# Optimization experiments

Measured on AMD Instinct MI355X. Metric: run time of the kernel, lower is better.

The kernel has to match this reference:

```python
import jax, jax.numpy as jnp
import numpy as np

N, K, NC = 1024, 32, 10
CH = (1, 4, 8, 32)
FT = (256, 64, 16, 1)
BN_EPS = 1e-5

def _sgnroot(a):
    return jnp.sign(a) * jnp.maximum(jnp.sqrt(jnp.abs(a)), 1e-8)

def _row_normalize(a):
    y = a / (jnp.sum(jnp.abs(a), -1, keepdims=True) + 1e-7)
    return jnp.where(jnp.isnan(y), 0.0, y)

def _feature_adjacency(x, nbr):
    # x: [N,C,F], nbr: [N,K,C,F] -> adj: [N,C,F,F]
    a = jnp.einsum('ncx,nkcy->ncxy', x, nbr)
    a = a + jnp.swapaxes(a, -1, -2)
    return _row_normalize(_sgnroot(a))

def _transform(x, nbr, adj, W, b, oc, of):
    # aggregate with feature adjacency, then full-width Conv1d == dense contraction
    xa = jnp.einsum('ncxy,ncy->ncx', adj, x)          # [N,C,F]
    na = jnp.einsum('ncxy,nkcy->nkcx', adj, nbr)      # [N,K,C,F]
    xo = (jnp.einsum('ncf,dcf->nd', xa, W) + b).reshape(-1, oc, of)
    no = (jnp.einsum('nkcf,dcf->nkd', na, W) + b).reshape(xo.shape[0], -1, oc, of)
    return xo, no

def _bn_softsign(v, g, be, m, var):
    # BatchNorm1d (inference, running stats) over channel axis -2, then Softsign
    h = (v - m[:, None]) * jax.lax.rsqrt(var[:, None] + BN_EPS) * g[:, None] + be[:, None]
    return h / (1.0 + jnp.abs(h))

def setup_inputs():
    key = jax.random.key(0)
    ks = jax.random.split(key, 24)
    def rn(i, shape, s=1.0):
        return jax.random.normal(ks[i], shape, dtype=jnp.float32) * s
    return {
        'x': rn(0, (N, CH[0], FT[0])),
        'neighbor': rn(1, (N, K, CH[0], FT[0])),
        'W1': rn(2, (CH[1] * FT[1], CH[0], FT[0]), 0.05), 'b1': rn(3, (CH[1] * FT[1],), 0.05),
        'g1': jnp.ones((CH[1],), jnp.float32), 'be1': jnp.zeros((CH[1],), jnp.float32),
        'm1': rn(4, (CH[1],), 0.1), 'v1': jax.random.uniform(ks[5], (CH[1],), jnp.float32) + 0.5,
        'W2': rn(6, (CH[2] * FT[2], CH[1], FT[1]), 0.05), 'b2': rn(7, (CH[2] * FT[2],), 0.05),
        'g2': jnp.ones((CH[2],), jnp.float32), 'be2': jnp.zeros((CH[2],), jnp.float32),
        'm2': rn(8, (CH[2],), 0.1), 'v2': jax.random.uniform(ks[9], (CH[2],), jnp.float32) + 0.5,
        'W3': rn(10, (CH[3] * FT[3], CH[2], FT[2]), 0.05), 'b3': rn(11, (CH[3] * FT[3],), 0.05),
        'g3': jnp.ones((CH[3],), jnp.float32), 'be3': jnp.zeros((CH[3],), jnp.float32),
        'm3': rn(12, (CH[3],), 0.1), 'v3': jax.random.uniform(ks[13], (CH[3],), jnp.float32) + 0.5,
        'Wc': rn(14, (NC, CH[3] * FT[3]), 0.1), 'bc': rn(15, (NC,), 0.1),
    }

def reference(x, neighbor, W1, b1, g1, be1, m1, v1, W2, b2, g2, be2, m2, v2,
              W3, b3, g3, be3, m3, v3, Wc, bc):
    adj = _feature_adjacency(x, neighbor)
    x, neighbor = _transform(x, neighbor, adj, W1, b1, CH[1], FT[1])
    x, neighbor = _bn_softsign(x, g1, be1, m1, v1), _bn_softsign(neighbor, g1, be1, m1, v1)
    adj = _feature_adjacency(x, neighbor)
    x, neighbor = _transform(x, neighbor, adj, W2, b2, CH[2], FT[2])
    x, neighbor = _bn_softsign(x, g2, be2, m2, v2), _bn_softsign(neighbor, g2, be2, m2, v2)
    adj = _feature_adjacency(x, neighbor)
    x, _ = _transform(x, neighbor, adj, W3, b3, CH[3], FT[3])
    x = _bn_softsign(x, g3, be3, m3, v3)
    return x.reshape(N, -1) @ Wc.T + bc
```

## Files before the change

kernel.cpp:

```cpp
#include <hip/hip_runtime.h>
#include <cstddef>

#define NPT 1024
#define KNB 32
#define NR  33

typedef __attribute__((ext_vector_type(8))) _Float16 half8v;
typedef __attribute__((ext_vector_type(4))) float float4v;
typedef __attribute__((ext_vector_type(2))) float float2v;

union fragU { unsigned u[4]; half8v v; };
union f4u { float4 f4; float2v f2[2]; };

__global__ __launch_bounds__(256) void wconv_kernel(
        const float* __restrict__ W1, const float* __restrict__ W2,
        _Float16* __restrict__ W1f, _Float16* __restrict__ W2f) {
    int idx = blockIdx.x * 256 + threadIdx.x;
    if (idx < 65536) W1f[idx] = (_Float16)W1[idx];
    else if (idx < 65536 + 32768) W2f[idx - 65536] = (_Float16)W2[idx - 65536];
}

template<int F>
__device__ __forceinline__ void agg_phase(
        const _Float16 (*Rh)[264], _Float16 (*Nh)[264],
        const float* Xs, const float* Ss, int wv, int lane) {
    const int nbase = wv * 64;
    const int kch = (nbase / F) * F;
    const int l15 = lane & 15, lg = lane >> 4;

    float Xn[4], Sn[4];
    #pragma unroll
    for (int i = 0; i < 4; ++i) {
        int col = nbase + i * 16 + l15;
        Xn[i] = Xs[col]; Sn[i] = Ss[col];
    }

    float4v acc[3][4] = {};
    float rn[4] = {0.f, 0.f, 0.f, 0.f};

    const int KT = F / 32;
    for (int kt = 0; kt < KT; ++kt) {
        const int k0 = kch + kt * 32 + lg * 8;
        half8v af[3];
        af[0] = *reinterpret_cast<const half8v*>(&Rh[l15][k0]);
        af[1] = *reinterpret_cast<const half8v*>(&Rh[16 + l15][k0]);
        af[2] = half8v{};
        if (l15 == 0)
            af[2] = *reinterpret_cast<const half8v*>(&Rh[32][k0]);
        f4u xa0, xa1, sa0, sa1;
        xa0.f4 = *reinterpret_cast<const float4*>(&Xs[k0]);
        xa1.f4 = *reinterpret_cast<const float4*>(&Xs[k0 + 4]);
        sa0.f4 = *reinterpret_cast<const float4*>(&Ss[k0]);
        sa1.f4 = *reinterpret_cast<const float4*>(&Ss[k0 + 4]);
        const float2v xk2[4] = {xa0.f2[0], xa0.f2[1], xa1.f2[0], xa1.f2[1]};
        const float2v sk2[4] = {sa0.f2[0], sa0.f2[1], sa1.f2[0], sa1.f2[1]};
        #pragma unroll
        for (int ni = 0; ni < 4; ++ni) {
            const float xn = Xn[ni], sn = Sn[ni];
            fragU bf;
            float2v rloc2 = {0.f, 0.f};
            #pragma unroll
            for (int jj = 0; jj < 4; ++jj) {
                const float2v a = xn * sk2[jj] + xk2[jj] * sn;
                const float r0 = __builtin_amdgcn_sqrtf(__builtin_fabsf(a.x));
                const float r1 = __builtin_amdgcn_sqrtf(__builtin_fabsf(a.y));
                rloc2 += (float2v){r0, r1};
                const unsigned mag = __builtin_bit_cast(unsigned,
                    __builtin_amdgcn_cvt_pkrtz(r0, r1));
                const unsigned sgn = __builtin_bit_cast(unsigned,
                    __builtin_amdgcn_cvt_pkrtz(a.x, a.y)) & 0x80008000u;
                bf.u[jj] = mag | sgn;
            }
            rn[ni] += rloc2.x + rloc2.y;
            #pragma unroll
            for (int m = 0; m < 3; ++m)
                acc[m][ni] = __builtin_amdgcn_mfma_f32_16x16x32_f16(
                                 af[m], bf.v, acc[m][ni], 0, 0, 0);
        }
    }

    #pragma unroll
    for (int ni = 0; ni < 4; ++ni) {
        rn[ni] += __shfl_xor(rn[ni], 16);
        rn[ni] += __shfl_xor(rn[ni], 32);
        rn[ni] = __builtin_amdgcn_rcpf(rn[ni] + 1e-7f);
    }

    #pragma unroll
    for (int m = 0; m < 3; ++m) {
        const int rbase = m * 16 + (lg << 2);
        #pragma unroll
        for (int ni = 0; ni < 4; ++ni) {
            const int col = nbase + ni * 16 + l15;
            #pragma unroll
            for (int i = 0; i < 4; ++i) {
                int r = rbase + i;
                if (r < NR)
                    Nh[r][col] = (_Float16)(acc[m][ni][i] * rn[ni]);
            }
        }
    }
}

template<int DOUT, int FP>
__device__ __forceinline__ void proj_phase(
        const _Float16 (*Nh)[264], _Float16 (*Rh)[264],
        float* Xs, float* Ss,
        const _Float16* __restrict__ Wf,
        const float* __restrict__ bias,
        const float* __restrict__ g, const float* __restrict__ be,
        const float* __restrict__ m, const float* __restrict__ var,
        int wv, int lane) {
    const int l15 = lane & 15, lg = lane >> 4;
    constexpr int NTW = DOUT / 64;
    const int nbase = wv * (NTW * 16);

    float4v acc[3][NTW] = {};

    for (int kt = 0; kt < 8; ++kt) {
        const int k0 = kt * 32 + lg * 8;
        half8v ah[3];
        ah[0] = *reinterpret_cast<const half8v*>(&Nh[l15][k0]);
        ah[1] = *reinterpret_cast<const half8v*>(&Nh[16 + l15][k0]);
        ah[2] = half8v{};
        if (l15 == 0)
            ah[2] = *reinterpret_cast<const half8v*>(&Nh[32][k0]);
        #pragma unroll
        for (int ni = 0; ni < NTW; ++ni) {
            const int d = nbase + ni * 16 + l15;
            const half8v bh = *reinterpret_cast<const half8v*>(Wf + (size_t)d * 256 + k0);
            #pragma unroll
            for (int mi = 0; mi < 3; ++mi)
                acc[mi][ni] = __builtin_amdgcn_mfma_f32_16x16x32_f16(
                                  ah[mi], bh, acc[mi][ni], 0, 0, 0);
        }
    }

    #pragma unroll
    for (int ni = 0; ni < NTW; ++ni) {
        const int col = nbase + ni * 16 + l15;
        const int c = (nbase + ni * 16) / FP;
        const float sc = g[c] * __builtin_amdgcn_rsqf(var[c] + 1e-5f);
        const float hb = (bias[col] - m[c]) * sc + be[c];
        float colsum = 0.f, xval = 0.f;
        #pragma unroll
        for (int mi = 0; mi < 3; ++mi) {
            const int rbase = mi * 16 + (lg << 2);
            #pragma unroll
            for (int i = 0; i < 4; ++i) {
                const int r = rbase + i;
                if (r < NR) {
                    float h = acc[mi][ni][i] * sc + hb;
                    h = h * __builtin_amdgcn_rcpf(1.f + __builtin_fabsf(h));
                    Rh[r][col] = (_Float16)h;
                    if (r < 32) colsum += h; else xval = h;
                }
            }
        }
        colsum += __shfl_xor(colsum, 16);
        colsum += __shfl_xor(colsum, 32);
        if (lg == 0) { Ss[col] = colsum; Xs[col] = xval; }
    }
}

__global__ __launch_bounds__(256, 4) void fused_kernel(
        const float* __restrict__ x, const float* __restrict__ nbr,
        const _Float16* __restrict__ W1f, const float* __restrict__ b1,
        const float* __restrict__ g1, const float* __restrict__ be1,
        const float* __restrict__ m1, const float* __restrict__ v1,
        const _Float16* __restrict__ W2f, const float* __restrict__ b2,
        const float* __restrict__ g2, const float* __restrict__ be2,
        const float* __restrict__ m2, const float* __restrict__ v2,
        const float* __restrict__ W3, const float* __restrict__ b3,
        const float* __restrict__ g3, const float* __restrict__ be3,
        const float* __restrict__ m3, const float* __restrict__ v3,
        const float* __restrict__ Wc, const float* __restrict__ bc,
        float* __restrict__ out) {
    const int n_pt = blockIdx.x, t = threadIdx.x;
    const int lane = t & 63, wv = t >> 6;

    __shared__ __align__(16) _Float16 Rh[NR][264];
    __shared__ __align__(16) _Float16 Nh[NR][264];
    __shared__ __align__(16) float Xs[256], Ss[256];
    __shared__ float xa3[128], hs3[32];

    {
        const float* nb = nbr + (size_t)n_pt * (KNB * 256);
        float s = 0.f;
        #pragma unroll 4
        for (int k = 0; k < KNB; ++k) {
            float v = nb[k * 256 + t];
            Rh[k][t] = (_Float16)v;
            s += v;
        }
        Ss[t] = s;
        float xv = x[(size_t)n_pt * 256 + t];
        Rh[32][t] = (_Float16)xv;
        Xs[t] = xv;
    }
    __syncthreads();

    agg_phase<256>(Rh, Nh, Xs, Ss, wv, lane);
    __syncthreads();
    proj_phase<256, 64>(Nh, Rh, Xs, Ss, W1f, b1, g1, be1, m1, v1, wv, lane);
    __syncthreads();

    agg_phase<64>(Rh, Nh, Xs, Ss, wv, lane);
    __syncthreads();
    proj_phase<128, 16>(Nh, Rh, Xs, Ss, W2f, b2, g2, be2, m2, v2, wv, lane);
    __syncthreads();

    if (t < 128) {
        const int base = (t >> 4) << 4;
        const float xv = Xs[t], sv = Ss[t];
        float racc = 0.f, acc = 0.f;
        #pragma unroll
        for (int y = 0; y < 16; ++y) {
            const float xy = Xs[base + y];
            const float a = xv * Ss[base + y] + xy * sv;
            const float r = __builtin_amdgcn_sqrtf(__builtin_fabsf(a));
            racc += r;
            acc += __builtin_copysignf(r, a) * xy;
        }
        xa3[t] = acc * __builtin_amdgcn_rcpf(racc + 1e-7f);
    }
    __syncthreads();

    if (t < 32) {
        const float* w = W3 + (size_t)t * 128;
        float acc = b3[t];
        #pragma unroll 4
        for (int i = 0; i < 128; ++i) acc += w[i] * xa3[i];
        float h = (acc - m3[t]) * __builtin_amdgcn_rsqf(v3[t] + 1e-5f) * g3[t] + be3[t];
        hs3[t] = h * __builtin_amdgcn_rcpf(1.f + __builtin_fabsf(h));
    }
    __syncthreads();

    if (t < 10) {
        const float* w = Wc + (size_t)t * 32;
        float acc = bc[t];
        #pragma unroll
        for (int i = 0; i < 32; ++i) acc += w[i] * hs3[i];
        out[(size_t)n_pt * 10 + t] = acc;
    }
}

extern "C" void kernel_launch(void* const* d_in, const int* in_sizes, int n_in,
                              void* d_out, int out_size, void* d_ws, size_t ws_size,
                              hipStream_t stream) {
    (void)in_sizes; (void)n_in; (void)out_size; (void)ws_size;
    const float* x   = (const float*)d_in[0];
    const float* nbr = (const float*)d_in[1];
    const float* W1  = (const float*)d_in[2];   const float* b1 = (const float*)d_in[3];
    const float* g1  = (const float*)d_in[4];   const float* be1 = (const float*)d_in[5];
    const float* m1  = (const float*)d_in[6];   const float* v1 = (const float*)d_in[7];
    const float* W2  = (const float*)d_in[8];   const float* b2 = (const float*)d_in[9];
    const float* g2  = (const float*)d_in[10];  const float* be2 = (const float*)d_in[11];
    const float* m2  = (const float*)d_in[12];  const float* v2 = (const float*)d_in[13];
    const float* W3  = (const float*)d_in[14];  const float* b3 = (const float*)d_in[15];
    const float* g3  = (const float*)d_in[16];  const float* be3 = (const float*)d_in[17];
    const float* m3  = (const float*)d_in[18];  const float* v3 = (const float*)d_in[19];
    const float* Wc  = (const float*)d_in[20];  const float* bc = (const float*)d_in[21];
    float* out = (float*)d_out;

    _Float16* W1f = (_Float16*)d_ws;
    _Float16* W2f = W1f + 65536;

    wconv_kernel<<<dim3((65536 + 32768 + 255) / 256), dim3(256), 0, stream>>>(
        W1, W2, W1f, W2f);
    fused_kernel<<<dim3(NPT), dim3(256), 0, stream>>>(
        x, nbr,
        W1f, b1, g1, be1, m1, v1,
        W2f, b2, g2, be2, m2, v2,
        W3, b3, g3, be3, m3, v3, Wc, bc, out);
}
```

Measured before the change: 51.09 us.

## Process two points per block with staggered phase pipeline across halves

Each 512-thread block now handles two points, with the second 256-thread group running one phase behind the first in a 9-slot loop that has one barrier per slot. The aim is to overlap dissimilar phases (global neighbor load, MFMA aggregation, projection, scalar tail) across the two groups so memory and compute work happen at the same time within a block. In exchange it adds an extra pipeline slot and doubles LDS per block, which may lower occupancy. Launch bounds drop from 4 blocks of 256 to 2 blocks of 512 per CU.

```diff
diff --git a/kernel.cpp b/kernel.cpp
--- a/kernel.cpp
+++ b/kernel.cpp
@@ -23,8 +23,8 @@
 template<int F>
 __device__ __forceinline__ void agg_phase(
         const _Float16 (*Rh)[264], _Float16 (*Nh)[264],
-        const float* Xs, const float* Ss, int wv, int lane) {
-    const int nbase = wv * 64;
+        const float* Xs, const float* Ss, int wl, int lane) {
+    const int nbase = wl * 64;
     const int kch = (nbase / F) * F;
     const int l15 = lane & 15, lg = lane >> 4;
 
@@ -110,10 +110,10 @@
         const float* __restrict__ bias,
         const float* __restrict__ g, const float* __restrict__ be,
         const float* __restrict__ m, const float* __restrict__ var,
-        int wv, int lane) {
+        int wl, int lane) {
     const int l15 = lane & 15, lg = lane >> 4;
     constexpr int NTW = DOUT / 64;
-    const int nbase = wv * (NTW * 16);
+    const int nbase = wl * (NTW * 16);
 
     float4v acc[3][NTW] = {};
 
@@ -163,7 +163,7 @@
     }
 }
 
-__global__ __launch_bounds__(256, 4) void fused_kernel(
+__global__ __launch_bounds__(512, 2) void fused_kernel(
         const float* __restrict__ x, const float* __restrict__ nbr,
         const _Float16* __restrict__ W1f, const float* __restrict__ b1,
         const float* __restrict__ g1, const float* __restrict__ be1,
@@ -176,72 +176,82 @@
         const float* __restrict__ m3, const float* __restrict__ v3,
         const float* __restrict__ Wc, const float* __restrict__ bc,
         float* __restrict__ out) {
-    const int n_pt = blockIdx.x, t = threadIdx.x;
-    const int lane = t & 63, wv = t >> 6;
-
-    __shared__ __align__(16) _Float16 Rh[NR][264];
-    __shared__ __align__(16) _Float16 Nh[NR][264];
-    __shared__ __align__(16) float Xs[256], Ss[256];
-    __shared__ float xa3[128], hs3[32];
-
-    {
-        const float* nb = nbr + (size_t)n_pt * (KNB * 256);
-        float s = 0.f;
-        #pragma unroll 4
-        for (int k = 0; k < KNB; ++k) {
-            float v = nb[k * 256 + t];
-            Rh[k][t] = (_Float16)v;
-            s += v;
-        }
-        Ss[t] = s;
-        float xv = x[(size_t)n_pt * 256 + t];
-        Rh[32][t] = (_Float16)xv;
-        Xs[t] = xv;
-    }
-    __syncthreads();
-
-    agg_phase<256>(Rh, Nh, Xs, Ss, wv, lane);
-    __syncthreads();
-    proj_phase<256, 64>(Nh, Rh, Xs, Ss, W1f, b1, g1, be1, m1, v1, wv, lane);
-    __syncthreads();
-
-    agg_phase<64>(Rh, Nh, Xs, Ss, wv, lane);
-    __syncthreads();
-    proj_phase<128, 16>(Nh, Rh, Xs, Ss, W2f, b2, g2, be2, m2, v2, wv, lane);
-    __syncthreads();
-
-    if (t < 128) {
-        const int base = (t >> 4) << 4;
-        const float xv = Xs[t], sv = Ss[t];
-        float racc = 0.f, acc = 0.f;
-        #pragma unroll
-        for (int y = 0; y < 16; ++y) {
-            const float xy = Xs[base + y];
-            const float a = xv * Ss[base + y] + xy * sv;
-            const float r = __builtin_amdgcn_sqrtf(__builtin_fabsf(a));
-            racc += r;
-            acc += __builtin_copysignf(r, a) * xy;
-        }
-        xa3[t] = acc * __builtin_amdgcn_rcpf(racc + 1e-7f);
-    }
-    __syncthreads();
-
-    if (t < 32) {
-        const float* w = W3 + (size_t)t * 128;
-        float acc = b3[t];
-        #pragma unroll 4
-        for (int i = 0; i < 128; ++i) acc += w[i] * xa3[i];
-        float h = (acc - m3[t]) * __builtin_amdgcn_rsqf(v3[t] + 1e-5f) * g3[t] + be3[t];
-        hs3[t] = h * __builtin_amdgcn_rcpf(1.f + __builtin_fabsf(h));
-    }
-    __syncthreads();
-
-    if (t < 10) {
-        const float* w = Wc + (size_t)t * 32;
-        float acc = bc[t];
-        #pragma unroll
-        for (int i = 0; i < 32; ++i) acc += w[i] * hs3[i];
-        out[(size_t)n_pt * 10 + t] = acc;
+    const int t = threadIdx.x;
+    const int grp = t >> 8;
+    const int tl = t & 255;
+    const int wl = tl >> 6;
+    const int lane = t & 63;
+    const int n_pt = blockIdx.x * 2 + grp;
+
+    __shared__ __align__(16) _Float16 Rh[2][NR][264];
+    __shared__ __align__(16) _Float16 Nh[2][NR][264];
+    __shared__ __align__(16) float Xs[2][256], Ss[2][256];
+    __shared__ float xa3[2][128], hs3[2][32];
+
+    _Float16 (*rh)[264] = Rh[grp];
+    _Float16 (*nh)[264] = Nh[grp];
+    float* xs = Xs[grp];
+    float* ss = Ss[grp];
+
+    #pragma unroll 1
+    for (int slot = 0; slot < 9; ++slot) {
+        const int p = slot - grp;
+        if (p == 0) {
+            const float* nb = nbr + (size_t)n_pt * (KNB * 256);
+            float s = 0.f;
+            #pragma unroll 4
+            for (int k = 0; k < KNB; ++k) {
+                float v = nb[k * 256 + tl];
+                rh[k][tl] = (_Float16)v;
+                s += v;
+            }
+            ss[tl] = s;
+            float xv = x[(size_t)n_pt * 256 + tl];
+            rh[32][tl] = (_Float16)xv;
+            xs[tl] = xv;
+        } else if (p == 1) {
+            agg_phase<256>(rh, nh, xs, ss, wl, lane);
+        } else if (p == 2) {
+            proj_phase<256, 64>(nh, rh, xs, ss, W1f, b1, g1, be1, m1, v1, wl, lane);
+        } else if (p == 3) {
+            agg_phase<64>(rh, nh, xs, ss, wl, lane);
+        } else if (p == 4) {
+            proj_phase<128, 16>(nh, rh, xs, ss, W2f, b2, g2, be2, m2, v2, wl, lane);
+        } else if (p == 5) {
+            if (tl < 128) {
+                const int base = (tl >> 4) << 4;
+                const float xv = xs[tl], sv = ss[tl];
+                float racc = 0.f, acc = 0.f;
+                #pragma unroll
+                for (int y = 0; y < 16; ++y) {
+                    const float xy = xs[base + y];
+                    const float a = xv * ss[base + y] + xy * sv;
+                    const float r = __builtin_amdgcn_sqrtf(__builtin_fabsf(a));
+                    racc += r;
+                    acc += __builtin_copysignf(r, a) * xy;
+                }
+                xa3[grp][tl] = acc * __builtin_amdgcn_rcpf(racc + 1e-7f);
+            }
+        } else if (p == 6) {
+            if (tl < 32) {
+                const float* w = W3 + (size_t)tl * 128;
+                float acc = b3[tl];
+                #pragma unroll 4
+                for (int i = 0; i < 128; ++i) acc += w[i] * xa3[grp][i];
+                float h = (acc - m3[tl]) * __builtin_amdgcn_rsqf(v3[tl] + 1e-5f)
+                              * g3[tl] + be3[tl];
+                hs3[grp][tl] = h * __builtin_amdgcn_rcpf(1.f + __builtin_fabsf(h));
+            }
+        } else if (p == 7) {
+            if (tl < 10) {
+                const float* w = Wc + (size_t)tl * 32;
+                float acc = bc[tl];
+                #pragma unroll
+                for (int i = 0; i < 32; ++i) acc += w[i] * hs3[grp][i];
+                out[(size_t)n_pt * 10 + tl] = acc;
+            }
+        }
+        __syncthreads();
     }
 }
 
@@ -268,7 +278,7 @@
 
     wconv_kernel<<<dim3((65536 + 32768 + 255) / 256), dim3(256), 0, stream>>>(
         W1, W2, W1f, W2f);
-    fused_kernel<<<dim3(NPT), dim3(256), 0, stream>>>(
+    fused_kernel<<<dim3(NPT / 2), dim3(512), 0, stream>>>(
         x, nbr,
         W1f, b1, g1, be1, m1, v1,
         W2f, b2, g2, be2, m2, v2,
```

New measurement: 78.15 us. +53.0%, slower.
